# Kernel optimization log

Hardware: AMD Instinct MI355X
Metric: run time of the kernel (lower is better)

Reference implementation:

```python
import jax, jax.numpy as jnp
import numpy as np

MAX_DEGREE = 5
NUM_LAYERS = 2


def setup_inputs() -> dict:
    key = jax.random.key(0)
    ks = jax.random.split(key, 10)
    N, F, H, C, E = 200000, 128, 64, 40, 3200000
    x = jax.random.normal(ks[0], (N, F), dtype=jnp.float32)
    edge_index = jax.random.randint(ks[1], (2, E), 0, N, dtype=jnp.int32)
    # torch Linear init ~ U(-1/sqrt(fan_in), 1/sqrt(fan_in)); scaled normals are fine for a baseline
    W1 = jax.random.normal(ks[2], (F, H), dtype=jnp.float32) / np.sqrt(F)
    b1 = jax.random.normal(ks[3], (H,), dtype=jnp.float32) * 0.01
    relW = jax.random.normal(ks[4], (NUM_LAYERS, MAX_DEGREE + 1, H, H), dtype=jnp.float32) / np.sqrt(H)
    relb = jax.random.normal(ks[5], (NUM_LAYERS, MAX_DEGREE + 1, H), dtype=jnp.float32) * 0.01
    Wout = jax.random.normal(ks[6], (H, C), dtype=jnp.float32) / np.sqrt(H)
    bout = jax.random.normal(ks[7], (C,), dtype=jnp.float32) * 0.01
    fuse = jnp.full((NUM_LAYERS,), 1.0 / (NUM_LAYERS + 1), dtype=jnp.float32)
    return {"x": x, "edge_index": edge_index, "W1": W1, "b1": b1,
            "relW": relW, "relb": relb, "Wout": Wout, "bout": bout, "fuse": fuse}


def reference(x, edge_index, W1, b1, relW, relb, Wout, bout, fuse):
    N = x.shape[0]
    src, dst = edge_index[0], edge_index[1]
    loop_mask = (src != dst)  # remove_self_loops
    # degree on target nodes (flow='source_to_target'), clamped to max_degree
    deg = jax.ops.segment_sum(loop_mask.astype(jnp.int32), dst, num_segments=N)
    deg = jnp.clip(deg, 0, MAX_DEGREE)
    node_idx = jnp.arange(N)

    h = jax.nn.relu(x @ W1 + b1)  # dropout is identity in eval mode
    x_first = h
    for i in range(NUM_LAYERS):
        # scatter-add aggregation; self loops added back (root_weight=False)
        msg = jnp.where(loop_mask[:, None], h[src], 0.0)  # [E, H]
        agg = jax.ops.segment_sum(msg, dst, num_segments=N) + h  # [N, H]
        # degree-bucketed linear: compute all 6 buckets, select per node
        all_out = jnp.einsum('nd,kdo->kno', agg, relW[i]) + relb[i][:, None, :]  # [6, N, H]
        conv = all_out[deg, node_idx]  # [N, H]
        h = conv + fuse[i] * x_first
    logits = h @ Wout + bout
    return jax.nn.log_softmax(logits, axis=-1)
```

## Files before the change

### kernel.cpp

```cpp
#include <hip/hip_runtime.h>
#include <cmath>
#include <cstddef>

#define F_IN 128
#define H_DIM 64
#define C_OUT 40
#define MAXDEG 5
#define EPB 16

typedef __attribute__((ext_vector_type(8))) _Float16 half8;
typedef __attribute__((ext_vector_type(4))) _Float16 half4;
typedef __attribute__((ext_vector_type(4))) float fv4;
typedef __attribute__((ext_vector_type(2))) float fv2;

__device__ __forceinline__ half4 u2h(uint2 u) { return __builtin_bit_cast(half4, u); }
__device__ __forceinline__ uint2 h2u(half4 v) { return __builtin_bit_cast(uint2, v); }
__device__ __forceinline__ half8 u2h8(uint4 u) { return __builtin_bit_cast(half8, u); }
__device__ __forceinline__ uint4 h2u8(half8 v) { return __builtin_bit_cast(uint4, v); }

__global__ __launch_bounds__(256) void k_scatter_lin1(
        const int* __restrict__ src, const int* __restrict__ dst,
        int E, int NB, int stride, int* __restrict__ gcnt,
        unsigned int* __restrict__ ebuf, int SB,
        const float* __restrict__ x, const float* __restrict__ W1,
        const float* __restrict__ b1,
        _Float16* __restrict__ h, _Float16* __restrict__ hz2,
        unsigned char* __restrict__ hq, unsigned char* __restrict__ hq2,
        int N, int ngroups) {
    __shared__ __align__(16) unsigned char smem_raw[16384];
    int tid = threadIdx.x;

    int bid = blockIdx.x;
    bool scat;
    int ridx;
    if (bid < 2 * SB) { scat = (bid & 1) == 0; ridx = bid >> 1; }
    else              { scat = false;          ridx = bid - SB; }

    if (scat) {
        int* hist = (int*)smem_raw;
        int* base = (int*)(smem_raw + 2048);
        for (int i = tid; i < NB; i += 256) hist[i] = 0;
        __syncthreads();
        int e0 = ridx * (256 * EPB);
        int es[EPB], ed[EPB];
#pragma unroll
        for (int i = 0; i < EPB; ++i) {
            int e = e0 + i * 256 + tid;
            int s = -1, d = -1;
            if (e < E) { s = src[e]; d = dst[e]; }
            es[i] = s; ed[i] = d;
            if (d >= 0 && s != d) atomicAdd(&hist[d >> 9], 1);
        }
        __syncthreads();
        for (int i = tid; i < NB; i += 256) {
            int c = hist[i];
            base[i] = c ? atomicAdd(&gcnt[i], c) : 0;
            hist[i] = 0;
        }
        __syncthreads();
#pragma unroll
        for (int i = 0; i < EPB; ++i) {
            int s = es[i], d = ed[i];
            if (d >= 0 && s != d) {
                int b = d >> 9;
                int p = base[b] + atomicAdd(&hist[b], 1);
                if (p < stride)
                    ebuf[(size_t)b * stride + p] = ((unsigned)(d & 511) << 20) | (unsigned)s;
            }
        }
        return;
    }

    _Float16* Wl = (_Float16*)smem_raw;
    int lb = ridx;
    int LG = gridDim.x - SB;
    if (lb == 0) {
        if (tid < 64) {
            h[(size_t)N * H_DIM + tid] = (_Float16)0.f;
            hz2[(size_t)N * H_DIM + tid] = (_Float16)0.f;
        }
        if (tid < 16) {
            ((unsigned*)(hq + (size_t)N * 64))[tid] = 0u;
            ((unsigned*)(hq2 + (size_t)N * 64))[tid] = 0u;
        }
    }
    for (int idx = tid; idx < 4 * 4 * 64 * 8; idx += 256) {
        int j = idx & 7, ln = (idx >> 3) & 63, ks = (idx >> 9) & 3, t = idx >> 11;
        int k = ks * 32 + (ln >> 4) * 8 + j;
        int n = t * 16 + (ln & 15);
        Wl[idx] = (_Float16)W1[k * H_DIM + n];
    }
    __syncthreads();

    int wave = tid >> 6, lane = tid & 63;
    int m = lane & 15, quad = lane >> 4;

    fv4 bb[4];
#pragma unroll
    for (int t = 0; t < 4; ++t)
        bb[t] = *(const fv4*)(b1 + t * 16 + quad * 4);

    for (int g = lb; g < ngroups; g += LG) {
        int row0 = g * 64 + wave * 16;
        int row = row0 + m;
        int rc = (row < N) ? row : (N - 1);

        half8 a[4];
        const float* xr = x + (size_t)rc * F_IN + quad * 8;
#pragma unroll
        for (int ks = 0; ks < 4; ++ks) {
            fv4 lo = *(const fv4*)(xr + ks * 32);
            fv4 hi = *(const fv4*)(xr + ks * 32 + 4);
            half8 av;
#pragma unroll
            for (int j = 0; j < 4; ++j) av[j] = (_Float16)lo[j];
#pragma unroll
            for (int j = 0; j < 4; ++j) av[4 + j] = (_Float16)hi[j];
            a[ks] = av;
        }

        fv4 acc[4];
#pragma unroll
        for (int t = 0; t < 4; ++t) acc[t] = (fv4){0.f, 0.f, 0.f, 0.f};
#pragma unroll
        for (int ks = 0; ks < 4; ++ks) {
#pragma unroll
            for (int t = 0; t < 4; ++t) {
                half8 b = *(const half8*)&Wl[(((t * 4 + ks) * 64) + lane) * 8];
                acc[t] = __builtin_amdgcn_mfma_f32_16x16x32_f16(b, a[ks], acc[t], 0, 0, 0);
            }
        }
        if (row < N) {
            _Float16* hr = h + (size_t)row * H_DIM;
            unsigned* hqr = (unsigned*)(hq) + (size_t)row * 16;
#pragma unroll
            for (int t = 0; t < 4; ++t) {
                float f[4];
                half4 hv;
#pragma unroll
                for (int reg = 0; reg < 4; ++reg) {
                    f[reg] = fmaxf(acc[t][reg] + bb[t][reg], 0.f);
                    hv[reg] = (_Float16)f[reg];
                }
                *reinterpret_cast<half4*>(hr + t * 16 + quad * 4) = hv;
                int q = __builtin_amdgcn_cvt_pk_fp8_f32(f[0], f[1], 0, 0);
                q = __builtin_amdgcn_cvt_pk_fp8_f32(f[2], f[3], q, 1);
                hqr[t * 4 + quad] = (unsigned)q;
            }
        }
    }
}

__global__ __launch_bounds__(512) void k_build(const unsigned int* __restrict__ ebuf,
                                               const int* __restrict__ gcnt, int stride, int N,
                                               int* __restrict__ row, int* __restrict__ cnt,
                                               int* __restrict__ col) {
    __shared__ int lcnt[512];
    __shared__ int lcur[512];
    int bk = blockIdx.x;
    int n0 = bk << 9;
    int tid = threadIdx.x;
    int ebase = bk * stride;
    int ec = min(gcnt[bk], stride);
    int eend = ebase + ec;
    lcnt[tid] = 0;
    __syncthreads();
    for (int e = ebase + tid; e < eend; e += 512)
        atomicAdd(&lcnt[ebuf[e] >> 20], 1);
    __syncthreads();
    int v = lcnt[tid];
    lcur[tid] = v;
    __syncthreads();
    for (int off = 1; off < 512; off <<= 1) {
        int t = (tid >= off) ? lcur[tid - off] : 0;
        __syncthreads();
        lcur[tid] += t;
        __syncthreads();
    }
    int ex = lcur[tid] - v;
    __syncthreads();
    lcur[tid] = ebase + ex;
    int n = n0 + tid;
    if (n < N) {
        row[n] = ebase + ex;
        cnt[n] = v;
    }
    __syncthreads();
    for (int e = ebase + tid; e < eend; e += 512) {
        unsigned edv = ebuf[e];
        int dl = edv >> 20;
        int p = atomicAdd(&lcur[dl], 1);
        col[p] = (int)(edv & 0xFFFFF);
    }
}

__global__ void k_agg(const _Float16* __restrict__ hin,
                      const unsigned char* __restrict__ hq,
                      const int* __restrict__ row,
                      const int* __restrict__ cnt, const int* __restrict__ col,
                      _Float16* __restrict__ agg, int N) {
    int wid = (blockIdx.x * blockDim.x + threadIdx.x) >> 6;
    int lane = threadIdx.x & 63;
    int g = lane >> 3, fl = lane & 7, gl = g << 3;
    int n = wid * 8 + g;
    bool nv = (n < N);
    int nn = nv ? n : (N - 1);
    int base = row[nn];
    int c = nv ? cnt[nn] : 0;
    const uint2* hv8 = (const uint2*)hq;
    int cmax = c;
    cmax = max(cmax, __shfl_xor(cmax, 8));
    cmax = max(cmax, __shfl_xor(cmax, 16));
    cmax = max(cmax, __shfl_xor(cmax, 32));
    float acc[8] = {0.f, 0.f, 0.f, 0.f, 0.f, 0.f, 0.f, 0.f};
    for (int j0 = 0; j0 < cmax; j0 += 8) {
        int idx = j0 + fl;
        int myc = (idx < c) ? col[base + idx] : N;
        int tmax = min(8, cmax - j0);
        if (tmax == 8) {
            uint2 u[8];
#pragma unroll
            for (int t = 0; t < 8; ++t) {
                int s = __shfl(myc, gl + t);
                u[t] = hv8[(size_t)s * 8 + fl];
            }
#pragma unroll
            for (int t = 0; t < 8; ++t) {
                fv2 p0 = __builtin_amdgcn_cvt_pk_f32_fp8((int)u[t].x, 0);
                fv2 p1 = __builtin_amdgcn_cvt_pk_f32_fp8((int)u[t].x, 1);
                fv2 p2 = __builtin_amdgcn_cvt_pk_f32_fp8((int)u[t].y, 0);
                fv2 p3 = __builtin_amdgcn_cvt_pk_f32_fp8((int)u[t].y, 1);
                acc[0] += p0[0]; acc[1] += p0[1]; acc[2] += p1[0]; acc[3] += p1[1];
                acc[4] += p2[0]; acc[5] += p2[1]; acc[6] += p3[0]; acc[7] += p3[1];
            }
        } else {
            for (int t = 0; t < tmax; ++t) {
                int s = __shfl(myc, gl + t);
                uint2 u = hv8[(size_t)s * 8 + fl];
                fv2 p0 = __builtin_amdgcn_cvt_pk_f32_fp8((int)u.x, 0);
                fv2 p1 = __builtin_amdgcn_cvt_pk_f32_fp8((int)u.x, 1);
                fv2 p2 = __builtin_amdgcn_cvt_pk_f32_fp8((int)u.y, 0);
                fv2 p3 = __builtin_amdgcn_cvt_pk_f32_fp8((int)u.y, 1);
                acc[0] += p0[0]; acc[1] += p0[1]; acc[2] += p1[0]; acc[3] += p1[1];
                acc[4] += p2[0]; acc[5] += p2[1]; acc[6] += p3[0]; acc[7] += p3[1];
            }
        }
    }
    const uint4* hv16 = (const uint4*)hin;
    half8 sh = u2h8(hv16[(size_t)nn * 8 + fl]);
#pragma unroll
    for (int i = 0; i < 8; ++i) acc[i] += (float)sh[i];
    if (nv) {
        half8 o;
#pragma unroll
        for (int i = 0; i < 8; ++i) o[i] = (_Float16)acc[i];
        ((uint4*)agg)[(size_t)nn * 8 + fl] = h2u8(o);
    }
}

__global__ __launch_bounds__(256) void k_bucket(const _Float16* __restrict__ agg,
                                                const int* __restrict__ cnt,
                                                const float* __restrict__ relW,
                                                const float* __restrict__ relb,
                                                const float* __restrict__ fuse, int layer,
                                                const _Float16* __restrict__ xfirst,
                                                _Float16* __restrict__ h,
                                                unsigned char* __restrict__ hq, int N) {
    __shared__ _Float16 Wl[4 * 2 * 64 * 8];
    __shared__ int flist[64];
    __shared__ int fn;
    const float* W = relW + (size_t)(layer * 6 + MAXDEG) * (H_DIM * H_DIM);
    int tid = threadIdx.x;
    if (tid == 0) fn = 0;
    for (int idx = tid; idx < 4 * 2 * 64 * 8; idx += 256) {
        int j = idx & 7, ln = (idx >> 3) & 63, ks = (idx >> 9) & 1, t = idx >> 10;
        int k = ks * 32 + (ln >> 4) * 8 + j;
        int n = t * 16 + (ln & 15);
        Wl[idx] = (_Float16)W[k * H_DIM + n];
    }
    __syncthreads();

    int wave = tid >> 6, lane = tid & 63;
    int row0 = blockIdx.x * 64 + wave * 16;
    int m = lane & 15, quad = lane >> 4;
    int row = row0 + m;
    int rc = (row < N) ? row : (N - 1);
    float fu = fuse[layer];
    const float* bias = relb + (layer * 6 + MAXDEG) * H_DIM;

    half8 a[2];
#pragma unroll
    for (int ks = 0; ks < 2; ++ks)
        a[ks] = *(const half8*)(agg + (size_t)rc * H_DIM + ks * 32 + quad * 8);

    fv4 acc[4];
#pragma unroll
    for (int t = 0; t < 4; ++t) acc[t] = (fv4){0.f, 0.f, 0.f, 0.f};
#pragma unroll
    for (int ks = 0; ks < 2; ++ks)
#pragma unroll
        for (int t = 0; t < 4; ++t) {
            half8 b = *(const half8*)&Wl[(((t * 2 + ks) * 64) + lane) * 8];
            acc[t] = __builtin_amdgcn_mfma_f32_16x16x32_f16(b, a[ks], acc[t], 0, 0, 0);
        }

    int c = (row < N) ? cnt[row] : MAXDEG;
    if (quad == 0 && row < N && c < MAXDEG) {
        int p = atomicAdd(&fn, 1);
        if (p < 64) flist[p] = wave * 16 + m;
    }
    if (row < N && c >= MAXDEG) {
        _Float16* hr = h + (size_t)row * H_DIM;
        unsigned* hqr = (unsigned*)(hq) + (size_t)row * 16;
        const _Float16* xr = xfirst + (size_t)row * H_DIM;
#pragma unroll
        for (int t = 0; t < 4; ++t) {
            fv4 bv = *(const fv4*)(bias + t * 16 + quad * 4);
            half4 xf = *reinterpret_cast<const half4*>(xr + t * 16 + quad * 4);
            float f[4];
            half4 hvv;
#pragma unroll
            for (int reg = 0; reg < 4; ++reg) {
                f[reg] = acc[t][reg] + bv[reg] + fu * (float)xf[reg];
                hvv[reg] = (_Float16)f[reg];
            }
            *reinterpret_cast<half4*>(hr + t * 16 + quad * 4) = hvv;
            int q = __builtin_amdgcn_cvt_pk_fp8_f32(f[0], f[1], 0, 0);
            q = __builtin_amdgcn_cvt_pk_fp8_f32(f[2], f[3], q, 1);
            hqr[t * 4 + quad] = (unsigned)q;
        }
    }
    __syncthreads();
    int M = min(fn, 64);
    for (int i = wave; i < M; i += 4) {
        int rl = flist[i];
        int r = blockIdx.x * 64 + rl;
        int d = cnt[r];
        const float* Wd = relW + (size_t)(layer * 6 + d) * (H_DIM * H_DIM);
        float av = (float)agg[(size_t)r * H_DIM + lane];
        float accf = relb[(layer * 6 + d) * H_DIM + lane];
        for (int k = 0; k < 64; ++k)
            accf = fmaf(__shfl(av, k), Wd[k * H_DIM + lane], accf);
        accf += fu * (float)xfirst[(size_t)r * H_DIM + lane];
        h[(size_t)r * H_DIM + lane] = (_Float16)accf;
        float a0 = __shfl(accf, lane & ~1);
        float a1 = __shfl(accf, lane | 1);
        if (!(lane & 1)) {
            int q = __builtin_amdgcn_cvt_pk_fp8_f32(a0, a1, 0, 0);
            ((unsigned short*)(hq + (size_t)r * 64))[lane >> 1] = (unsigned short)(q & 0xFFFF);
        }
    }
}

#define HB 80
__global__ __launch_bounds__(256) void k_bucket_out(const _Float16* __restrict__ agg,
                                                    const int* __restrict__ cnt,
                                                    const float* __restrict__ relW,
                                                    const float* __restrict__ relb,
                                                    const float* __restrict__ fuse,
                                                    const _Float16* __restrict__ xfirst,
                                                    const float* __restrict__ Wout,
                                                    const float* __restrict__ bout,
                                                    float* __restrict__ out, int N) {
    __shared__ _Float16 Wl[4 * 2 * 64 * 8];
    __shared__ _Float16 Wo[3 * 2 * 64 * 8];
    __shared__ _Float16 hbuf[64 * HB];
    __shared__ int flist[64];
    __shared__ int fn;
    const int layer = 1;
    const float* W = relW + (size_t)(layer * 6 + MAXDEG) * (H_DIM * H_DIM);
    int tid = threadIdx.x;
    if (tid == 0) fn = 0;
    for (int idx = tid; idx < 4 * 2 * 64 * 8; idx += 256) {
        int j = idx & 7, ln = (idx >> 3) & 63, ks = (idx >> 9) & 1, t = idx >> 10;
        int k = ks * 32 + (ln >> 4) * 8 + j;
        int n = t * 16 + (ln & 15);
        Wl[idx] = (_Float16)W[k * H_DIM + n];
    }
    for (int idx = tid; idx < 3 * 2 * 64 * 8; idx += 256) {
        int j = idx & 7, ln = (idx >> 3) & 63, ks = (idx >> 9) & 1, t = idx >> 10;
        int k = ks * 32 + (ln >> 4) * 8 + j;
        int n = t * 16 + (ln & 15);
        Wo[idx] = (n < C_OUT) ? (_Float16)Wout[k * C_OUT + n] : (_Float16)0.f;
    }
    __syncthreads();

    int wave = tid >> 6, lane = tid & 63;
    int row0 = blockIdx.x * 64 + wave * 16;
    int m = lane & 15, quad = lane >> 4;
    int row = row0 + m;
    int rc = (row < N) ? row : (N - 1);
    float fu = fuse[layer];
    const float* bias = relb + (layer * 6 + MAXDEG) * H_DIM;

    half8 a[2];
#pragma unroll
    for (int ks = 0; ks < 2; ++ks)
        a[ks] = *(const half8*)(agg + (size_t)rc * H_DIM + ks * 32 + quad * 8);

    fv4 acc[4];
#pragma unroll
    for (int t = 0; t < 4; ++t) acc[t] = (fv4){0.f, 0.f, 0.f, 0.f};
#pragma unroll
    for (int ks = 0; ks < 2; ++ks)
#pragma unroll
        for (int t = 0; t < 4; ++t) {
            half8 b = *(const half8*)&Wl[(((t * 2 + ks) * 64) + lane) * 8];
            acc[t] = __builtin_amdgcn_mfma_f32_16x16x32_f16(b, a[ks], acc[t], 0, 0, 0);
        }

    int c = (row < N) ? cnt[row] : MAXDEG;
    if (quad == 0 && row < N && c < MAXDEG) {
        int p = atomicAdd(&fn, 1);
        if (p < 64) flist[p] = wave * 16 + m;
    }
    {
        int rl = wave * 16 + m;
        const _Float16* xr = xfirst + (size_t)rc * H_DIM;
#pragma unroll
        for (int t = 0; t < 4; ++t) {
            fv4 bv = *(const fv4*)(bias + t * 16 + quad * 4);
            half4 xf = *reinterpret_cast<const half4*>(xr + t * 16 + quad * 4);
            half4 hvv;
#pragma unroll
            for (int reg = 0; reg < 4; ++reg)
                hvv[reg] = (_Float16)(acc[t][reg] + bv[reg] + fu * (float)xf[reg]);
            *reinterpret_cast<half4*>(&hbuf[rl * HB + t * 16 + quad * 4]) = hvv;
        }
    }
    __syncthreads();
    int M = min(fn, 64);
    for (int i = wave; i < M; i += 4) {
        int rl = flist[i];
        int r = blockIdx.x * 64 + rl;
        int d = cnt[r];
        const float* Wd = relW + (size_t)(layer * 6 + d) * (H_DIM * H_DIM);
        float av = (float)agg[(size_t)r * H_DIM + lane];
        float accf = relb[(layer * 6 + d) * H_DIM + lane];
        for (int k = 0; k < 64; ++k)
            accf = fmaf(__shfl(av, k), Wd[k * H_DIM + lane], accf);
        accf += fu * (float)xfirst[(size_t)r * H_DIM + lane];
        hbuf[rl * HB + lane] = (_Float16)accf;
    }
    __syncthreads();

    half8 ao[2];
#pragma unroll
    for (int ks = 0; ks < 2; ++ks)
        ao[ks] = *(const half8*)&hbuf[(wave * 16 + m) * HB + ks * 32 + quad * 8];

    fv4 lacc[3];
#pragma unroll
    for (int t = 0; t < 3; ++t) lacc[t] = (fv4){0.f, 0.f, 0.f, 0.f};
#pragma unroll
    for (int ks = 0; ks < 2; ++ks)
#pragma unroll
        for (int t = 0; t < 3; ++t) {
            half8 b = *(const half8*)&Wo[(((t * 2 + ks) * 64) + lane) * 8];
            lacc[t] = __builtin_amdgcn_mfma_f32_16x16x32_f16(ao[ks], b, lacc[t], 0, 0, 0);
        }
    bool v2 = (m < 8);
    float b0 = bout[m], b1v = bout[16 + m], b2v = v2 ? bout[32 + m] : 0.f;
#pragma unroll
    for (int reg = 0; reg < 4; ++reg) {
        int r = row0 + quad * 4 + reg;
        float l0 = lacc[0][reg] + b0;
        float l1 = lacc[1][reg] + b1v;
        float l2 = v2 ? (lacc[2][reg] + b2v) : -INFINITY;
        float mx = fmaxf(fmaxf(l0, l1), l2);
#pragma unroll
        for (int off = 1; off < 16; off <<= 1) mx = fmaxf(mx, __shfl_xor(mx, off));
        float s = expf(l0 - mx) + expf(l1 - mx) + (v2 ? expf(l2 - mx) : 0.f);
#pragma unroll
        for (int off = 1; off < 16; off <<= 1) s += __shfl_xor(s, off);
        float ls = logf(s);
        if (r < N) {
            out[(size_t)r * C_OUT + m] = l0 - mx - ls;
            out[(size_t)r * C_OUT + 16 + m] = l1 - mx - ls;
            if (v2) out[(size_t)r * C_OUT + 32 + m] = l2 - mx - ls;
        }
    }
}

extern "C" void kernel_launch(void* const* d_in, const int* in_sizes, int n_in,
                              void* d_out, int out_size, void* d_ws, size_t ws_size,
                              hipStream_t stream) {
    const float* x    = (const float*)d_in[0];
    const int*   ei   = (const int*)d_in[1];
    const float* W1   = (const float*)d_in[2];
    const float* b1   = (const float*)d_in[3];
    const float* relW = (const float*)d_in[4];
    const float* relb = (const float*)d_in[5];
    const float* Wout = (const float*)d_in[6];
    const float* bout = (const float*)d_in[7];
    const float* fuse = (const float*)d_in[8];
    float* out = (float*)d_out;

    int N = in_sizes[0] / F_IN;
    int E = in_sizes[1] / 2;
    const int* src = ei;
    const int* dst = ei + E;
    int NB = (N + 511) >> 9;
    int mean = (E + NB - 1) / NB;
    int stride = mean + mean / 8 + 512;

    char* w = (char*)d_ws;
    auto alloc = [&](size_t bytes) {
        char* p = w;
        w += (bytes + 255) & ~(size_t)255;
        return p;
    };
    int* cnt  = (int*)alloc((size_t)N * 4);
    int* row  = (int*)alloc((size_t)N * 4);
    int* gcnt = (int*)alloc(1024 * 4);
    int* col  = (int*)alloc((size_t)NB * stride * 4);
    _Float16* h0   = (_Float16*)alloc((size_t)(N + 1) * H_DIM * 2);
    _Float16* h1   = (_Float16*)alloc((size_t)(N + 1) * H_DIM * 2);
    _Float16* aggb = (_Float16*)alloc((size_t)N * H_DIM * 2);
    unsigned char* h0q = (unsigned char*)alloc((size_t)(N + 1) * 64);
    unsigned char* h1q = (unsigned char*)alloc((size_t)(N + 1) * 64);
    unsigned int* ebuf = (unsigned int*)alloc((size_t)NB * stride * 4);

    hipMemsetAsync(gcnt, 0, 1024 * 4, stream);

    int sblk = (E + 256 * EPB - 1) / (256 * EPB);
    int ngroups = (N + 63) / 64;
    int lgrid = ngroups < 1024 ? ngroups : 1024;
    k_scatter_lin1<<<sblk + lgrid, 256, 0, stream>>>(src, dst, E, NB, stride, gcnt, ebuf,
                                                     sblk, x, W1, b1, h0, h1, h0q, h1q,
                                                     N, ngroups);
    k_build<<<NB, 512, 0, stream>>>(ebuf, gcnt, stride, N, row, cnt, col);

    int tiles = (N + 15) / 16;
    int gblk = (tiles + 3) / 4;
    int awaves = (N + 7) / 8;
    int ablk = (awaves * 64 + 255) / 256;

    k_agg<<<ablk, 256, 0, stream>>>(h0, h0q, row, cnt, col, aggb, N);
    k_bucket<<<gblk, 256, 0, stream>>>(aggb, cnt, relW, relb, fuse, 0, h0, h1, h1q, N);

    k_agg<<<ablk, 256, 0, stream>>>(h1, h1q, row, cnt, col, aggb, N);
    k_bucket_out<<<gblk, 256, 0, stream>>>(aggb, cnt, relW, relb, fuse, h0, Wout, bout, out, N);
}
```

Baseline: 430.0 us.

## Fuse neighbor aggregation into degree-bucketed linear kernels via shared-memory tile

The separate aggregation kernel is merged into both bucket kernels. Each block now gathers and sums the neighbor features for its 64 rows directly into a padded shared-memory tile, which the MFMA linear step reads instead of a global agg buffer. This removes the global agg round trip and two kernel launches per forward pass. In exchange, each block runs a longer gather phase before its matmul, adds shared memory per block that may lower occupancy, and leaves less room to hide gather latency than the standalone aggregation kernel had.

```diff
diff --git a/kernel.cpp b/kernel.cpp
--- a/kernel.cpp
+++ b/kernel.cpp
@@ -7,6 +7,7 @@
 #define C_OUT 40
 #define MAXDEG 5
 #define EPB 16
+#define AGS 72
 
 typedef __attribute__((ext_vector_type(8))) _Float16 half8;
 typedef __attribute__((ext_vector_type(4))) _Float16 half4;
@@ -194,20 +195,18 @@
     }
 }
 
-__global__ void k_agg(const _Float16* __restrict__ hin,
-                      const unsigned char* __restrict__ hq,
-                      const int* __restrict__ row,
-                      const int* __restrict__ cnt, const int* __restrict__ col,
-                      _Float16* __restrict__ agg, int N) {
-    int wid = (blockIdx.x * blockDim.x + threadIdx.x) >> 6;
-    int lane = threadIdx.x & 63;
-    int g = lane >> 3, fl = lane & 7, gl = g << 3;
-    int n = wid * 8 + g;
+__device__ __forceinline__ void agg8(const _Float16* __restrict__ hin,
+                                     const unsigned char* __restrict__ hqin,
+                                     const int* __restrict__ row,
+                                     const int* __restrict__ cnt,
+                                     const int* __restrict__ col,
+                                     _Float16* aggt, int rl, int n, int N,
+                                     int fl, int gl) {
     bool nv = (n < N);
     int nn = nv ? n : (N - 1);
     int base = row[nn];
     int c = nv ? cnt[nn] : 0;
-    const uint2* hv8 = (const uint2*)hq;
+    const uint2* hv8 = (const uint2*)hqin;
     int cmax = c;
     cmax = max(cmax, __shfl_xor(cmax, 8));
     cmax = max(cmax, __shfl_xor(cmax, 16));
@@ -246,27 +245,23 @@
             }
         }
     }
-    const uint4* hv16 = (const uint4*)hin;
-    half8 sh = u2h8(hv16[(size_t)nn * 8 + fl]);
-#pragma unroll
-    for (int i = 0; i < 8; ++i) acc[i] += (float)sh[i];
-    if (nv) {
-        half8 o;
-#pragma unroll
-        for (int i = 0; i < 8; ++i) o[i] = (_Float16)acc[i];
-        ((uint4*)agg)[(size_t)nn * 8 + fl] = h2u8(o);
-    }
+    half8 sh = u2h8(((const uint4*)hin)[(size_t)nn * 8 + fl]);
+    half8 o;
+#pragma unroll
+    for (int i = 0; i < 8; ++i) o[i] = (_Float16)(acc[i] + (float)sh[i]);
+    *reinterpret_cast<half8*>(&aggt[rl * AGS + fl * 8]) = o;
 }
 
-__global__ __launch_bounds__(256) void k_bucket(const _Float16* __restrict__ agg,
-                                                const int* __restrict__ cnt,
-                                                const float* __restrict__ relW,
-                                                const float* __restrict__ relb,
-                                                const float* __restrict__ fuse, int layer,
-                                                const _Float16* __restrict__ xfirst,
-                                                _Float16* __restrict__ h,
-                                                unsigned char* __restrict__ hq, int N) {
+__global__ __launch_bounds__(256) void k_agg_bucket(
+        const _Float16* __restrict__ hin, const unsigned char* __restrict__ hqin,
+        const int* __restrict__ row, const int* __restrict__ cnt,
+        const int* __restrict__ col,
+        const float* __restrict__ relW, const float* __restrict__ relb,
+        const float* __restrict__ fuse, int layer,
+        const _Float16* __restrict__ xfirst,
+        _Float16* __restrict__ h, unsigned char* __restrict__ hqout, int N) {
     __shared__ _Float16 Wl[4 * 2 * 64 * 8];
+    __shared__ _Float16 aggt[64 * AGS];
     __shared__ int flist[64];
     __shared__ int fn;
     const float* W = relW + (size_t)(layer * 6 + MAXDEG) * (H_DIM * H_DIM);
@@ -278,20 +273,27 @@
         int n = t * 16 + (ln & 15);
         Wl[idx] = (_Float16)W[k * H_DIM + n];
     }
-    __syncthreads();
-
     int wave = tid >> 6, lane = tid & 63;
+    {
+        int g = lane >> 3, fl = lane & 7, gl = g << 3;
+#pragma unroll
+        for (int half = 0; half < 2; ++half) {
+            int rl = wave * 16 + half * 8 + g;
+            agg8(hin, hqin, row, cnt, col, aggt, rl, blockIdx.x * 64 + rl, N, fl, gl);
+        }
+    }
+    __syncthreads();
+
     int row0 = blockIdx.x * 64 + wave * 16;
     int m = lane & 15, quad = lane >> 4;
-    int row = row0 + m;
-    int rc = (row < N) ? row : (N - 1);
+    int rrow = row0 + m;
     float fu = fuse[layer];
     const float* bias = relb + (layer * 6 + MAXDEG) * H_DIM;
 
     half8 a[2];
 #pragma unroll
     for (int ks = 0; ks < 2; ++ks)
-        a[ks] = *(const half8*)(agg + (size_t)rc * H_DIM + ks * 32 + quad * 8);
+        a[ks] = *(const half8*)&aggt[(wave * 16 + m) * AGS + ks * 32 + quad * 8];
 
     fv4 acc[4];
 #pragma unroll
@@ -304,15 +306,15 @@
             acc[t] = __builtin_amdgcn_mfma_f32_16x16x32_f16(b, a[ks], acc[t], 0, 0, 0);
         }
 
-    int c = (row < N) ? cnt[row] : MAXDEG;
-    if (quad == 0 && row < N && c < MAXDEG) {
+    int c = (rrow < N) ? cnt[rrow] : MAXDEG;
+    if (quad == 0 && rrow < N && c < MAXDEG) {
         int p = atomicAdd(&fn, 1);
         if (p < 64) flist[p] = wave * 16 + m;
     }
-    if (row < N && c >= MAXDEG) {
-        _Float16* hr = h + (size_t)row * H_DIM;
-        unsigned* hqr = (unsigned*)(hq) + (size_t)row * 16;
-        const _Float16* xr = xfirst + (size_t)row * H_DIM;
+    if (rrow < N && c >= MAXDEG) {
+        _Float16* hr = h + (size_t)rrow * H_DIM;
+        unsigned* hqr = (unsigned*)(hqout) + (size_t)rrow * 16;
+        const _Float16* xr = xfirst + (size_t)rrow * H_DIM;
 #pragma unroll
         for (int t = 0; t < 4; ++t) {
             fv4 bv = *(const fv4*)(bias + t * 16 + quad * 4);
@@ -337,7 +339,7 @@
         int r = blockIdx.x * 64 + rl;
         int d = cnt[r];
         const float* Wd = relW + (size_t)(layer * 6 + d) * (H_DIM * H_DIM);
-        float av = (float)agg[(size_t)r * H_DIM + lane];
+        float av = (float)aggt[rl * AGS + lane];
         float accf = relb[(layer * 6 + d) * H_DIM + lane];
         for (int k = 0; k < 64; ++k)
             accf = fmaf(__shfl(av, k), Wd[k * H_DIM + lane], accf);
@@ -347,24 +349,25 @@
         float a1 = __shfl(accf, lane | 1);
         if (!(lane & 1)) {
             int q = __builtin_amdgcn_cvt_pk_fp8_f32(a0, a1, 0, 0);
-            ((unsigned short*)(hq + (size_t)r * 64))[lane >> 1] = (unsigned short)(q & 0xFFFF);
+            ((unsigned short*)(hqout + (size_t)r * 64))[lane >> 1] = (unsigned short)(q & 0xFFFF);
         }
     }
 }
 
 #define HB 80
-__global__ __launch_bounds__(256) void k_bucket_out(const _Float16* __restrict__ agg,
-                                                    const int* __restrict__ cnt,
-                                                    const float* __restrict__ relW,
-                                                    const float* __restrict__ relb,
-                                                    const float* __restrict__ fuse,
-                                                    const _Float16* __restrict__ xfirst,
-                                                    const float* __restrict__ Wout,
-                                                    const float* __restrict__ bout,
-                                                    float* __restrict__ out, int N) {
+__global__ __launch_bounds__(256) void k_agg_bucket_out(
+        const _Float16* __restrict__ hin, const unsigned char* __restrict__ hqin,
+        const int* __restrict__ row, const int* __restrict__ cnt,
+        const int* __restrict__ col,
+        const float* __restrict__ relW, const float* __restrict__ relb,
+        const float* __restrict__ fuse,
+        const _Float16* __restrict__ xfirst,
+        const float* __restrict__ Wout, const float* __restrict__ bout,
+        float* __restrict__ out, int N) {
     __shared__ _Float16 Wl[4 * 2 * 64 * 8];
     __shared__ _Float16 Wo[3 * 2 * 64 * 8];
     __shared__ _Float16 hbuf[64 * HB];
+    __shared__ _Float16 aggt[64 * AGS];
     __shared__ int flist[64];
     __shared__ int fn;
     const int layer = 1;
@@ -383,20 +386,28 @@
         int n = t * 16 + (ln & 15);
         Wo[idx] = (n < C_OUT) ? (_Float16)Wout[k * C_OUT + n] : (_Float16)0.f;
     }
-    __syncthreads();
-
     int wave = tid >> 6, lane = tid & 63;
+    {
+        int g = lane >> 3, fl = lane & 7, gl = g << 3;
+#pragma unroll
+        for (int half = 0; half < 2; ++half) {
+            int rl = wave * 16 + half * 8 + g;
+            agg8(hin, hqin, row, cnt, col, aggt, rl, blockIdx.x * 64 + rl, N, fl, gl);
+        }
+    }
+    __syncthreads();
+
     int row0 = blockIdx.x * 64 + wave * 16;
     int m = lane & 15, quad = lane >> 4;
-    int row = row0 + m;
-    int rc = (row < N) ? row : (N - 1);
+    int rrow = row0 + m;
+    int rc = (rrow < N) ? rrow : (N - 1);
     float fu = fuse[layer];
     const float* bias = relb + (layer * 6 + MAXDEG) * H_DIM;
 
     half8 a[2];
 #pragma unroll
     for (int ks = 0; ks < 2; ++ks)
-        a[ks] = *(const half8*)(agg + (size_t)rc * H_DIM + ks * 32 + quad * 8);
+        a[ks] = *(const half8*)&aggt[(wave * 16 + m) * AGS + ks * 32 + quad * 8];
 
     fv4 acc[4];
 #pragma unroll
@@ -409,8 +420,8 @@
             acc[t] = __builtin_amdgcn_mfma_f32_16x16x32_f16(b, a[ks], acc[t], 0, 0, 0);
         }
 
-    int c = (row < N) ? cnt[row] : MAXDEG;
-    if (quad == 0 && row < N && c < MAXDEG) {
+    int c = (rrow < N) ? cnt[rrow] : MAXDEG;
+    if (quad == 0 && rrow < N && c < MAXDEG) {
         int p = atomicAdd(&fn, 1);
         if (p < 64) flist[p] = wave * 16 + m;
     }
@@ -435,7 +446,7 @@
         int r = blockIdx.x * 64 + rl;
         int d = cnt[r];
         const float* Wd = relW + (size_t)(layer * 6 + d) * (H_DIM * H_DIM);
-        float av = (float)agg[(size_t)r * H_DIM + lane];
+        float av = (float)aggt[rl * AGS + lane];
         float accf = relb[(layer * 6 + d) * H_DIM + lane];
         for (int k = 0; k < 64; ++k)
             accf = fmaf(__shfl(av, k), Wd[k * H_DIM + lane], accf);
@@ -516,7 +527,6 @@
     int* col  = (int*)alloc((size_t)NB * stride * 4);
     _Float16* h0   = (_Float16*)alloc((size_t)(N + 1) * H_DIM * 2);
     _Float16* h1   = (_Float16*)alloc((size_t)(N + 1) * H_DIM * 2);
-    _Float16* aggb = (_Float16*)alloc((size_t)N * H_DIM * 2);
     unsigned char* h0q = (unsigned char*)alloc((size_t)(N + 1) * 64);
     unsigned char* h1q = (unsigned char*)alloc((size_t)(N + 1) * 64);
     unsigned int* ebuf = (unsigned int*)alloc((size_t)NB * stride * 4);
@@ -531,14 +541,9 @@
                                                      N, ngroups);
     k_build<<<NB, 512, 0, stream>>>(ebuf, gcnt, stride, N, row, cnt, col);
 
-    int tiles = (N + 15) / 16;
-    int gblk = (tiles + 3) / 4;
-    int awaves = (N + 7) / 8;
-    int ablk = (awaves * 64 + 255) / 256;
-
-    k_agg<<<ablk, 256, 0, stream>>>(h0, h0q, row, cnt, col, aggb, N);
-    k_bucket<<<gblk, 256, 0, stream>>>(aggb, cnt, relW, relb, fuse, 0, h0, h1, h1q, N);
-
-    k_agg<<<ablk, 256, 0, stream>>>(h1, h1q, row, cnt, col, aggb, N);
-    k_bucket_out<<<gblk, 256, 0, stream>>>(aggb, cnt, relW, relb, fuse, h0, Wout, bout, out, N);
+    int gblk = (N + 63) / 64;
+    k_agg_bucket<<<gblk, 256, 0, stream>>>(h0, h0q, row, cnt, col, relW, relb, fuse, 0,
+                                           h0, h1, h1q, N);
+    k_agg_bucket_out<<<gblk, 256, 0, stream>>>(h1, h1q, row, cnt, col, relW, relb, fuse,
+                                               h0, Wout, bout, out, N);
 }
```

New measurement: 432.1 us. About the same (+0.5%).
